# Optimization experiments

Hardware: AMD Instinct MI355X
Metric: run time of the kernel (lower is better)

## Reference

```python
import jax, jax.numpy as jnp
import numpy as np

TOP_K = 8
ROUTED_SCALING_FACTOR = 2.5
NORM_TOPK_PROB = True


def setup_inputs() -> dict:
    key = jax.random.key(0)
    k1, k2 = jax.random.split(key)
    hidden_states = jax.random.normal(k1, (4, 4096, 4096), dtype=jnp.float32)
    # gate weight: (n_routed_experts, hidden_size)
    weight = jax.random.normal(k2, (256, 4096), dtype=jnp.float32) * (1.0 / np.sqrt(4096))
    return {"hidden_states": hidden_states, "weight": weight}


def reference(hidden_states, weight):
    bsz, seq_len, h = hidden_states.shape
    x = hidden_states.reshape(-1, h).astype(jnp.float32)  # [T, h]
    # gate logits: [T, E]
    logits = jnp.einsum("th,eh->te", x, weight.astype(jnp.float32))
    scores = jax.nn.softmax(logits, axis=-1)
    topk_weight, topk_idx = jax.lax.top_k(scores, TOP_K)  # [T, k]
    if TOP_K > 1 and NORM_TOPK_PROB:
        denom = jnp.sum(topk_weight, axis=-1, keepdims=True) + 1e-20
        topk_weight = topk_weight / denom * ROUTED_SCALING_FACTOR
    else:
        topk_weight = topk_weight * ROUTED_SCALING_FACTOR
    return (topk_idx, topk_weight)
```

## Files before the change

kernel.cpp:

```cpp
#include <hip/hip_runtime.h>
#include <math.h>

typedef _Float16 half8  __attribute__((ext_vector_type(8)));
typedef _Float16 half4v __attribute__((ext_vector_type(4)));
typedef float    f32x16 __attribute__((ext_vector_type(16)));

namespace {
constexpr int H      = 4096;
constexpr int E      = 256;
constexpr int TOPK   = 8;
constexpr int NCAND  = 12;
constexpr int BM     = 64;
constexpr int NCHUNK = H / 32;
constexpr int SLD    = E + 4;
constexpr float DELTA = 5e-4f;
constexpr size_t WF_BYTES = (size_t)E * H * 2 * 2;
}

__global__ void convert_w_kernel(const float* __restrict__ W,
                                 _Float16* __restrict__ Wf) {
    int t  = blockIdx.x * blockDim.x + threadIdx.x;
    int e  = t >> 10;
    int kq = t & 1023;
    float4 w4 = *(const float4*)(W + ((size_t)e << 12) + (kq << 2));
    float x0 = w4.x * 64.0f, x1 = w4.y * 64.0f, x2 = w4.z * 64.0f, x3 = w4.w * 64.0f;
    _Float16 h0 = (_Float16)x0, h1 = (_Float16)x1, h2 = (_Float16)x2, h3 = (_Float16)x3;
    _Float16 l0 = (_Float16)(x0 - (float)h0), l1 = (_Float16)(x1 - (float)h1);
    _Float16 l2 = (_Float16)(x2 - (float)h2), l3 = (_Float16)(x3 - (float)h3);
    int k    = kq << 2;
    int nt   = e >> 5;
    int ks   = k >> 4;
    int lane = (e & 31) | (((k >> 3) & 1) << 5);
    int j    = k & 7;
    size_t base = (((size_t)nt * 256 + ks) * 2) * 512 + lane * 8 + j;
    half4v hv = {h0, h1, h2, h3};
    half4v lv = {l0, l1, l2, l3};
    *(half4v*)(Wf + base)       = hv;
    *(half4v*)(Wf + base + 512) = lv;
}

__global__ __launch_bounds__(512, 2)
void moe_gate_mfma(const float* __restrict__ X, const _Float16* __restrict__ Wf,
                   const float* __restrict__ Wg,
                   float* __restrict__ out_idx, float* __restrict__ out_w) {
    __shared__ float sc[BM * SLD];

    const int tid  = threadIdx.x;
    const int lane = tid & 63;
    const int wave = tid >> 6;
    const int wr   = wave >> 2;
    const int wc   = wave & 3;
    const int m0   = blockIdx.x * BM;

    const float*    ap = X + (size_t)(m0 + wr * 32 + (lane & 31)) * H + ((lane >> 5) * 8);
    const _Float16* bp = Wf + lane * 8;

    f32x16 acc[2];
    #pragma unroll
    for (int nt = 0; nt < 2; ++nt)
        #pragma unroll
        for (int r = 0; r < 16; ++r) acc[nt][r] = 0.0f;

    float4 af[2][2][2];
    half8  bh[2][2][2], bl[2][2][2];

    auto load_a = [&](int kc, int buf) {
        #pragma unroll
        for (int ks = 0; ks < 2; ++ks) {
            const float* p = ap + kc * 32 + ks * 16;
            af[buf][ks][0] = *(const float4*)(p);
            af[buf][ks][1] = *(const float4*)(p + 4);
        }
    };
    auto load_bf = [&](int kc, int buf) {
        #pragma unroll
        for (int ks = 0; ks < 2; ++ks)
            #pragma unroll
            for (int nt = 0; nt < 2; ++nt) {
                const _Float16* p = bp
                    + (((size_t)(2 * wc + nt) * 256 + (kc * 2 + ks)) * 2) * 512;
                bh[buf][ks][nt] = *(const half8*)(p);
                bl[buf][ks][nt] = *(const half8*)(p + 512);
            }
    };

    load_a(0, 0);
    load_bf(0, 0);

    #pragma unroll 2
    for (int kc = 0; kc < NCHUNK; ++kc) {
        const int cur = kc & 1, nxt = cur ^ 1;
        const int kn  = (kc + 1 < NCHUNK) ? kc + 1 : kc;
        load_a(kn, nxt);
        load_bf(kn, nxt);
        #pragma unroll
        for (int ks = 0; ks < 2; ++ks) {
            float xr[8];
            *(float4*)&xr[0] = af[cur][ks][0];
            *(float4*)&xr[4] = af[cur][ks][1];
            half8 a_hi, a_lo;
            #pragma unroll
            for (int j = 0; j < 8; ++j) {
                _Float16 h = (_Float16)xr[j];
                a_hi[j] = h;
                a_lo[j] = (_Float16)(xr[j] - (float)h);
            }
            #pragma unroll
            for (int nt = 0; nt < 2; ++nt) {
                acc[nt] = __builtin_amdgcn_mfma_f32_32x32x16_f16(a_hi, bh[cur][ks][nt], acc[nt], 0, 0, 0);
                acc[nt] = __builtin_amdgcn_mfma_f32_32x32x16_f16(a_lo, bh[cur][ks][nt], acc[nt], 0, 0, 0);
                acc[nt] = __builtin_amdgcn_mfma_f32_32x32x16_f16(a_hi, bl[cur][ks][nt], acc[nt], 0, 0, 0);
            }
        }
    }

    #pragma unroll
    for (int nt = 0; nt < 2; ++nt) {
        #pragma unroll
        for (int r = 0; r < 16; ++r) {
            int row = (r & 3) + 8 * (r >> 2) + 4 * (lane >> 5);
            int col = lane & 31;
            sc[(wr * 32 + row) * SLD + wc * 64 + nt * 32 + col] = acc[nt][r] * 0.015625f;
        }
    }
    __syncthreads();

    for (int t8 = 0; t8 < 8; ++t8) {
        const int t = wave * 8 + t8;
        float4 pv = *(const float4*)(sc + t * SLD + lane * 4);
        float p0 = pv.x, p1 = pv.y, p2 = pv.z, p3 = pv.w;

        float tv[NCAND]; int ti[NCAND];
        #pragma unroll
        for (int s = 0; s < NCAND; ++s) {
            float bv = p0; int bi = lane * 4;
            if (p1 > bv || (p1 == bv && lane * 4 + 1 < bi)) { bv = p1; bi = lane * 4 + 1; }
            if (p2 > bv || (p2 == bv && lane * 4 + 2 < bi)) { bv = p2; bi = lane * 4 + 2; }
            if (p3 > bv || (p3 == bv && lane * 4 + 3 < bi)) { bv = p3; bi = lane * 4 + 3; }
            #pragma unroll
            for (int off = 32; off > 0; off >>= 1) {
                float ov = __shfl_xor(bv, off, 64);
                int   oi = __shfl_xor(bi, off, 64);
                if (ov > bv || (ov == bv && oi < bi)) { bv = ov; bi = oi; }
            }
            tv[s] = bv; ti[s] = bi;
            if ((bi >> 2) == lane) {
                const int sl = bi & 3;
                if      (sl == 0) p0 = -3e38f;
                else if (sl == 1) p1 = -3e38f;
                else if (sl == 2) p2 = -3e38f;
                else              p3 = -3e38f;
            }
        }

        bool rescue = false;
        #pragma unroll
        for (int g = 0; g < 9; ++g) rescue |= (tv[g] - tv[g + 1] < DELTA);

        if (rescue) {
            double dv[NCAND];
            const float* xr = X + (size_t)(m0 + t) * H;
            #pragma unroll 1
            for (int c = 0; c < NCAND; ++c) {
                const float* wrow = Wg + (size_t)ti[c] * H;
                double s_ = 0.0;
                #pragma unroll
                for (int it = 0; it < 16; ++it) {
                    float4 xa = *(const float4*)(xr + it * 256 + lane * 4);
                    float4 wa = *(const float4*)(wrow + it * 256 + lane * 4);
                    s_ += (double)xa.x * wa.x + (double)xa.y * wa.y
                        + (double)xa.z * wa.z + (double)xa.w * wa.w;
                }
                #pragma unroll
                for (int off = 32; off > 0; off >>= 1) s_ += __shfl_xor(s_, off, 64);
                dv[c] = s_;
            }
            int si[NCAND];
            #pragma unroll
            for (int c = 0; c < NCAND; ++c) si[c] = ti[c];
            #pragma unroll
            for (int a = 0; a < TOPK; ++a) {
                int best = a;
                #pragma unroll
                for (int b = a + 1; b < NCAND; ++b) {
                    if (dv[b] > dv[best] || (dv[b] == dv[best] && si[b] < si[best])) best = b;
                }
                double tdv = dv[a]; dv[a] = dv[best]; dv[best] = tdv;
                int    tsi = si[a]; si[a] = si[best]; si[best] = tsi;
            }
            #pragma unroll
            for (int s = 0; s < TOPK; ++s) { tv[s] = (float)dv[s]; ti[s] = si[s]; }
        }

        if (lane == 0) {
            float M = tv[0];
            float e8[TOPK]; float den = 0.0f;
            #pragma unroll
            for (int s = 0; s < TOPK; ++s) { e8[s] = expf(tv[s] - M); den += e8[s]; }
            float scl = 2.5f / den;
            size_t tok = (size_t)(m0 + t);
            #pragma unroll
            for (int s = 0; s < TOPK; ++s) {
                out_idx[tok * TOPK + s] = (float)ti[s];
                out_w[tok * TOPK + s]   = e8[s] * scl;
            }
        }
    }
}

namespace fb {
constexpr int BM = 32, BK = 32;
constexpr int XS_LD = BM + 4, WS_LD = E + 4;
constexpr int LDS_FLOATS = BK * XS_LD + BK * WS_LD;
}

__global__ __launch_bounds__(256, 2)
void moe_gate_fallback(const float* __restrict__ X, const float* __restrict__ W,
                       float* __restrict__ out_idx, float* __restrict__ out_w) {
    __shared__ float lds[fb::LDS_FLOATS];
    float* xs = lds;
    float* ws = lds + fb::BK * fb::XS_LD;
    const int tid = threadIdx.x;
    const int tx = tid & 31, ty = tid >> 5;
    const int m0 = blockIdx.x * fb::BM;
    float acc[4][8];
    #pragma unroll
    for (int i = 0; i < 4; ++i)
        #pragma unroll
        for (int j = 0; j < 8; ++j) acc[i][j] = 0.0f;
    const int lr = tid >> 3, lc = (tid & 7) * 4;
    const float* xg = X + (size_t)(m0 + lr) * H + lc;
    const float* wg = W + (size_t)lr * H + lc;
    for (int kc = 0; kc < H; kc += fb::BK) {
        float4 xv = *(const float4*)(xg + kc);
        float4 wv[8];
        #pragma unroll
        for (int i = 0; i < 8; ++i) wv[i] = *(const float4*)(wg + (size_t)i * 32 * H + kc);
        __syncthreads();
        #pragma unroll
        for (int j = 0; j < 4; ++j) xs[(lc + j) * fb::XS_LD + lr] = ((const float*)&xv)[j];
        #pragma unroll
        for (int i = 0; i < 8; ++i)
            #pragma unroll
            for (int j = 0; j < 4; ++j)
                ws[(lc + j) * fb::WS_LD + i * 32 + lr] = ((const float*)&wv[i])[j];
        __syncthreads();
        #pragma unroll
        for (int kk = 0; kk < fb::BK; ++kk) {
            float4 xa = *(const float4*)(xs + kk * fb::XS_LD + ty * 4);
            float4 wb0 = *(const float4*)(ws + kk * fb::WS_LD + tx * 8);
            float4 wb1 = *(const float4*)(ws + kk * fb::WS_LD + tx * 8 + 4);
            const float xr[4] = {xa.x, xa.y, xa.z, xa.w};
            const float wr8[8] = {wb0.x, wb0.y, wb0.z, wb0.w, wb1.x, wb1.y, wb1.z, wb1.w};
            #pragma unroll
            for (int i = 0; i < 4; ++i)
                #pragma unroll
                for (int j = 0; j < 8; ++j) acc[i][j] = fmaf(xr[i], wr8[j], acc[i][j]);
        }
    }
    __syncthreads();
    float* sc = lds;
    #pragma unroll
    for (int i = 0; i < 4; ++i) {
        *(float4*)(sc + (ty * 4 + i) * fb::WS_LD + tx * 8) =
            make_float4(acc[i][0], acc[i][1], acc[i][2], acc[i][3]);
        *(float4*)(sc + (ty * 4 + i) * fb::WS_LD + tx * 8 + 4) =
            make_float4(acc[i][4], acc[i][5], acc[i][6], acc[i][7]);
    }
    __syncthreads();
    const int wave = tid >> 6, lane = tid & 63;
    for (int t8 = 0; t8 < 8; ++t8) {
        const int t = wave * 8 + t8;
        float4 pv = *(const float4*)(sc + t * fb::WS_LD + lane * 4);
        float v0 = pv.x, v1 = pv.y, v2 = pv.z, v3 = pv.w;
        float M = fmaxf(fmaxf(v0, v1), fmaxf(v2, v3));
        #pragma unroll
        for (int off = 32; off > 0; off >>= 1) M = fmaxf(M, __shfl_xor(M, off, 64));
        float p0 = expf(v0 - M), p1 = expf(v1 - M), p2 = expf(v2 - M), p3 = expf(v3 - M);
        float z = p0 + p1 + p2 + p3;
        #pragma unroll
        for (int off = 32; off > 0; off >>= 1) z += __shfl_xor(z, off, 64);
        p0 /= z; p1 /= z; p2 /= z; p3 /= z;
        float tv[TOPK]; int ti[TOPK];
        #pragma unroll
        for (int s = 0; s < TOPK; ++s) {
            float bv = p0; int bi = lane * 4;
            if (p1 > bv || (p1 == bv && lane * 4 + 1 < bi)) { bv = p1; bi = lane * 4 + 1; }
            if (p2 > bv || (p2 == bv && lane * 4 + 2 < bi)) { bv = p2; bi = lane * 4 + 2; }
            if (p3 > bv || (p3 == bv && lane * 4 + 3 < bi)) { bv = p3; bi = lane * 4 + 3; }
            #pragma unroll
            for (int off = 32; off > 0; off >>= 1) {
                float ov = __shfl_xor(bv, off, 64);
                int   oi = __shfl_xor(bi, off, 64);
                if (ov > bv || (ov == bv && oi < bi)) { bv = ov; bi = oi; }
            }
            tv[s] = bv; ti[s] = bi;
            if ((bi >> 2) == lane) {
                const int sl = bi & 3;
                if      (sl == 0) p0 = -1.0f;
                else if (sl == 1) p1 = -1.0f;
                else if (sl == 2) p2 = -1.0f;
                else              p3 = -1.0f;
            }
        }
        if (lane == 0) {
            float den = tv[0] + tv[1] + tv[2] + tv[3] + tv[4] + tv[5] + tv[6] + tv[7] + 1e-20f;
            float scl = 2.5f / den;
            size_t tok = (size_t)(m0 + t);
            #pragma unroll
            for (int s = 0; s < TOPK; ++s) {
                out_idx[tok * TOPK + s] = (float)ti[s];
                out_w[tok * TOPK + s]   = tv[s] * scl;
            }
        }
    }
}

extern "C" void kernel_launch(void* const* d_in, const int* in_sizes, int n_in,
                              void* d_out, int out_size, void* d_ws, size_t ws_size,
                              hipStream_t stream) {
    const float* X = (const float*)d_in[0];
    const float* W = (const float*)d_in[1];
    float* out = (float*)d_out;
    const int T = in_sizes[0] / H;
    float* out_idx = out;
    float* out_w   = out + (size_t)T * TOPK;

    if (ws_size >= WF_BYTES && (T % BM) == 0) {
        _Float16* Wf = (_Float16*)d_ws;
        hipLaunchKernelGGL(convert_w_kernel, dim3((E * (H / 4)) / 256), dim3(256), 0, stream, W, Wf);
        hipLaunchKernelGGL(moe_gate_mfma, dim3(T / BM), dim3(512), 0, stream, X, Wf, W, out_idx, out_w);
    } else {
        hipLaunchKernelGGL(moe_gate_fallback, dim3(T / fb::BM), dim3(256), 0, stream, X, W, out_idx, out_w);
    }
}
```

Before: 734.5 us.

## Shrink token tile to 32 rows with one 32-expert column per wave

Halves the block's token tile from 64 to 32 rows. Each of the 8 waves now computes a single 32x32 output tile covering 32 experts instead of two tiles, and launch bounds are raised to target 4 blocks per CU. This doubles the grid size and cuts per-wave registers, which should improve occupancy and latency hiding. In exchange, each block re-reads the full converted weight matrix for half as many tokens, doubling weight traffic relative to the activation loads.

Measured after the change: 912.3 us. +24.2%, slower.

```diff
diff --git a/kernel.cpp b/kernel.cpp
--- a/kernel.cpp
+++ b/kernel.cpp
@@ -10,7 +10,7 @@
 constexpr int E      = 256;
 constexpr int TOPK   = 8;
 constexpr int NCAND  = 12;
-constexpr int BM     = 64;
+constexpr int BM     = 32;
 constexpr int NCHUNK = H / 32;
 constexpr int SLD    = E + 4;
 constexpr float DELTA = 5e-4f;
@@ -39,7 +39,7 @@
     *(half4v*)(Wf + base + 512) = lv;
 }
 
-__global__ __launch_bounds__(512, 2)
+__global__ __launch_bounds__(512, 4)
 void moe_gate_mfma(const float* __restrict__ X, const _Float16* __restrict__ Wf,
                    const float* __restrict__ Wg,
                    float* __restrict__ out_idx, float* __restrict__ out_w) {
@@ -48,21 +48,17 @@
     const int tid  = threadIdx.x;
     const int lane = tid & 63;
     const int wave = tid >> 6;
-    const int wr   = wave >> 2;
-    const int wc   = wave & 3;
     const int m0   = blockIdx.x * BM;
 
-    const float*    ap = X + (size_t)(m0 + wr * 32 + (lane & 31)) * H + ((lane >> 5) * 8);
+    const float*    ap = X + (size_t)(m0 + (lane & 31)) * H + ((lane >> 5) * 8);
     const _Float16* bp = Wf + lane * 8;
 
-    f32x16 acc[2];
+    f32x16 acc;
     #pragma unroll
-    for (int nt = 0; nt < 2; ++nt)
-        #pragma unroll
-        for (int r = 0; r < 16; ++r) acc[nt][r] = 0.0f;
+    for (int r = 0; r < 16; ++r) acc[r] = 0.0f;
 
     float4 af[2][2][2];
-    half8  bh[2][2][2], bl[2][2][2];
+    half8  bh[2][2], bl[2][2];
 
     auto load_a = [&](int kc, int buf) {
         #pragma unroll
@@ -74,14 +70,12 @@
     };
     auto load_bf = [&](int kc, int buf) {
         #pragma unroll
-        for (int ks = 0; ks < 2; ++ks)
-            #pragma unroll
-            for (int nt = 0; nt < 2; ++nt) {
-                const _Float16* p = bp
-                    + (((size_t)(2 * wc + nt) * 256 + (kc * 2 + ks)) * 2) * 512;
-                bh[buf][ks][nt] = *(const half8*)(p);
-                bl[buf][ks][nt] = *(const half8*)(p + 512);
-            }
+        for (int ks = 0; ks < 2; ++ks) {
+            const _Float16* p = bp
+                + (((size_t)wave * 256 + (kc * 2 + ks)) * 2) * 512;
+            bh[buf][ks] = *(const half8*)(p);
+            bl[buf][ks] = *(const half8*)(p + 512);
+        }
     };
 
     load_a(0, 0);
@@ -105,28 +99,22 @@
                 a_hi[j] = h;
                 a_lo[j] = (_Float16)(xr[j] - (float)h);
             }
-            #pragma unroll
-            for (int nt = 0; nt < 2; ++nt) {
-                acc[nt] = __builtin_amdgcn_mfma_f32_32x32x16_f16(a_hi, bh[cur][ks][nt], acc[nt], 0, 0, 0);
-                acc[nt] = __builtin_amdgcn_mfma_f32_32x32x16_f16(a_lo, bh[cur][ks][nt], acc[nt], 0, 0, 0);
-                acc[nt] = __builtin_amdgcn_mfma_f32_32x32x16_f16(a_hi, bl[cur][ks][nt], acc[nt], 0, 0, 0);
-            }
+            acc = __builtin_amdgcn_mfma_f32_32x32x16_f16(a_hi, bh[cur][ks], acc, 0, 0, 0);
+            acc = __builtin_amdgcn_mfma_f32_32x32x16_f16(a_lo, bh[cur][ks], acc, 0, 0, 0);
+            acc = __builtin_amdgcn_mfma_f32_32x32x16_f16(a_hi, bl[cur][ks], acc, 0, 0, 0);
         }
     }
 
     #pragma unroll
-    for (int nt = 0; nt < 2; ++nt) {
-        #pragma unroll
-        for (int r = 0; r < 16; ++r) {
-            int row = (r & 3) + 8 * (r >> 2) + 4 * (lane >> 5);
-            int col = lane & 31;
-            sc[(wr * 32 + row) * SLD + wc * 64 + nt * 32 + col] = acc[nt][r] * 0.015625f;
-        }
+    for (int r = 0; r < 16; ++r) {
+        int row = (r & 3) + 8 * (r >> 2) + 4 * (lane >> 5);
+        int col = lane & 31;
+        sc[row * SLD + wave * 32 + col] = acc[r] * 0.015625f;
     }
     __syncthreads();
 
-    for (int t8 = 0; t8 < 8; ++t8) {
-        const int t = wave * 8 + t8;
+    for (int t8 = 0; t8 < 4; ++t8) {
+        const int t = wave * 4 + t8;
         float4 pv = *(const float4*)(sc + t * SLD + lane * 4);
         float p0 = pv.x, p1 = pv.y, p2 = pv.z, p3 = pv.w;
 
```
